# Performance work log

Measured on AMD Instinct MI355X. Metric: run time of the kernel, lower is better.

Reference implementation:

```python
import jax, jax.numpy as jnp
import numpy as np

SHAPES = ((100, 100), (50, 50), (25, 25), (13, 13))
LENS = [h * w for h, w in SHAPES]
STARTS = [0]
for n in LENS[:-1]:
    STARTS.append(STARTS[-1] + n)
S_TOT = sum(LENS)  # 13294
B, C, HH, DH, L, P, NQ, NL, FF = 2, 256, 8, 32, 4, 4, 300, 6, 1024
WH = np.array([[w, h] for h, w in SHAPES], np.float32)  # [L,2] (W,H) offset normalizer


def ln(x, g, b):
    m = x.mean(-1, keepdims=True)
    v = ((x - m) ** 2).mean(-1, keepdims=True)
    return (x - m) * jax.lax.rsqrt(v + 1e-5) * g + b


def bilinear(v, grid):
    # v: [N,Hl,Wl,D]; grid: [N,Q,2] in [-1,1]; grid_sample bilinear, align_corners=False, zero padding
    N, Hl, Wl, Dd = v.shape
    x = (grid[..., 0] + 1.0) * 0.5 * Wl - 0.5
    y = (grid[..., 1] + 1.0) * 0.5 * Hl - 0.5
    x0f = jnp.floor(x); y0f = jnp.floor(y)
    wx = x - x0f; wy = y - y0f
    x0 = x0f.astype(jnp.int32); y0 = y0f.astype(jnp.int32)
    vf = v.reshape(N, Hl * Wl, Dd)
    def g(yi, xi):
        valid = (yi >= 0) & (yi < Hl) & (xi >= 0) & (xi < Wl)
        idx = jnp.clip(yi, 0, Hl - 1) * Wl + jnp.clip(xi, 0, Wl - 1)
        return jnp.take_along_axis(vf, idx[..., None], axis=1) * valid[..., None]
    return (((1 - wy) * (1 - wx))[..., None] * g(y0, x0)
            + ((1 - wy) * wx)[..., None] * g(y0, x0 + 1)
            + (wy * (1 - wx))[..., None] * g(y0 + 1, x0)
            + (wy * wx)[..., None] * g(y0 + 1, x0 + 1))


def msda(query, ref, src, so_w, so_b, aw_w, aw_b, vp_w, vp_b, op_w, op_b):
    # query:[B,Lq,C] ref:[B,Lq,L,2] src:[B,S,C]
    Bq, Lq, _ = query.shape
    value = (src @ vp_w.T + vp_b).reshape(Bq, S_TOT, HH, DH)
    offs = (query @ so_w.T + so_b).reshape(Bq, Lq, HH, L, P, 2)
    aw = jax.nn.softmax((query @ aw_w.T + aw_b).reshape(Bq, Lq, HH, L * P), -1)
    aw = aw.reshape(Bq, Lq, HH, L, P)
    loc = ref[:, :, None, :, None, :] + offs / jnp.asarray(WH)[None, None, None, :, None, :]
    grid = 2.0 * loc - 1.0  # [B,Lq,HH,L,P,2]
    out = jnp.zeros((Bq, HH, Lq, DH), query.dtype)
    for l, (Hl, Wl) in enumerate(SHAPES):
        st = STARTS[l]
        v_l = value[:, st:st + Hl * Wl].reshape(Bq, Hl, Wl, HH, DH).transpose(0, 3, 1, 2, 4).reshape(Bq * HH, Hl, Wl, DH)
        g_l = grid[:, :, :, l].transpose(0, 2, 1, 3, 4).reshape(Bq * HH, Lq * P, 2)
        s = bilinear(v_l, g_l).reshape(Bq, HH, Lq, P, DH)
        out = out + jnp.einsum('bqhp,bhqpd->bhqd', aw[:, :, :, l], s)
    out = out.transpose(0, 2, 1, 3).reshape(Bq, Lq, C)
    return out @ op_w.T + op_b


def enc_ref_points():
    refs = []
    for Hl, Wl in SHAPES:
        ry = (jnp.arange(Hl, dtype=jnp.float32) + 0.5) / Hl
        rx = (jnp.arange(Wl, dtype=jnp.float32) + 0.5) / Wl
        gy, gx = jnp.meshgrid(ry, rx, indexing='ij')
        refs.append(jnp.stack([gx.reshape(-1), gy.reshape(-1)], -1))
    r = jnp.concatenate(refs, 0)  # [S,2]; valid_ratios == 1 (no padding)
    return jnp.broadcast_to(r[None, :, None, :], (B, S_TOT, L, 2))


def _forward(src_flatten, pos_flatten, query_embed, level_embed, refp_w, refp_b,
             eso_w, eso_b, eaw_w, eaw_b, evp_w, evp_b, eop_w, eop_b,
             en1_g, en1_b, el1_w, el1_b, el2_w, el2_b, en2_g, en2_b,
             dso_w, dso_b, daw_w, daw_b, dvp_w, dvp_b, dop_w, dop_b,
             dsa_in_w, dsa_in_b, dsa_out_w, dsa_out_b,
             dn1_g, dn1_b, dn2_g, dn2_b, dn3_g, dn3_b,
             dl1_w, dl1_b, dl2_w, dl2_b):
    lev = jnp.concatenate([jnp.broadcast_to(level_embed[l], (LENS[l], C)) for l in range(L)], 0)
    pos = pos_flatten + lev[None]
    memory = src_flatten
    eref = enc_ref_points()
    for i in range(NL):  # encoder
        q = memory + pos
        m2 = msda(q, eref, memory, eso_w[i], eso_b[i], eaw_w[i], eaw_b[i], evp_w[i], evp_b[i], eop_w[i], eop_b[i])
        memory = ln(memory + m2, en1_g[i], en1_b[i])
        f = jax.nn.relu(memory @ el1_w[i].T + el1_b[i]) @ el2_w[i].T + el2_b[i]
        memory = ln(memory + f, en2_g[i], en2_b[i])
    qpos, tgt = jnp.split(query_embed, 2, axis=-1)
    qpos = jnp.broadcast_to(qpos[None], (B, NQ, C))
    tgt = jnp.broadcast_to(tgt[None], (B, NQ, C))
    ref = jax.nn.sigmoid(qpos @ refp_w.T + refp_b)  # [B,NQ,2]
    init_ref = ref
    ref_in = jnp.broadcast_to(ref[:, :, None, :], (B, NQ, L, 2))
    scale = 1.0 / np.sqrt(DH)
    for i in range(NL):  # decoder
        q = tgt + qpos
        wq, wk, wv = jnp.split(dsa_in_w[i], 3, 0)
        bq, bk, bv = jnp.split(dsa_in_b[i], 3, 0)
        qh = (q @ wq.T + bq).reshape(B, NQ, HH, DH).transpose(0, 2, 1, 3)
        kh = (q @ wk.T + bk).reshape(B, NQ, HH, DH).transpose(0, 2, 1, 3)
        vh = (tgt @ wv.T + bv).reshape(B, NQ, HH, DH).transpose(0, 2, 1, 3)
        att = jax.nn.softmax(jnp.einsum('bhqd,bhkd->bhqk', qh, kh) * scale, -1)
        sa = jnp.einsum('bhqk,bhkd->bhqd', att, vh).transpose(0, 2, 1, 3).reshape(B, NQ, C)
        sa = sa @ dsa_out_w[i].T + dsa_out_b[i]
        tgt = ln(tgt + sa, dn2_g[i], dn2_b[i])
        ca = msda(tgt + qpos, ref_in, memory, dso_w[i], dso_b[i], daw_w[i], daw_b[i], dvp_w[i], dvp_b[i], dop_w[i], dop_b[i])
        tgt = ln(tgt + ca, dn1_g[i], dn1_b[i])
        f = jax.nn.relu(tgt @ dl1_w[i].T + dl1_b[i]) @ dl2_w[i].T + dl2_b[i]
        tgt = ln(tgt + f, dn3_g[i], dn3_b[i])
    return tgt, init_ref, ref


def setup_inputs() -> dict:
    ks = iter(jax.random.split(jax.random.key(0), 80))
    def rn(shape, s=0.02):
        return jax.random.normal(next(ks), shape, jnp.float32) * s
    z = lambda shape: jnp.zeros(shape, jnp.float32)
    o = lambda shape: jnp.ones(shape, jnp.float32)
    HLP2, HLP = HH * L * P * 2, HH * L * P
    return {
        'src_flatten': rn((B, S_TOT, C), 1.0),
        'pos_flatten': rn((B, S_TOT, C), 1.0),
        'query_embed': rn((NQ, 2 * C), 1.0),
        'level_embed': rn((L, C), 1.0),
        'refp_w': rn((2, C)), 'refp_b': z((2,)),
        'eso_w': rn((NL, HLP2, C)), 'eso_b': z((NL, HLP2)),
        'eaw_w': rn((NL, HLP, C)), 'eaw_b': z((NL, HLP)),
        'evp_w': rn((NL, C, C)), 'evp_b': z((NL, C)),
        'eop_w': rn((NL, C, C)), 'eop_b': z((NL, C)),
        'en1_g': o((NL, C)), 'en1_b': z((NL, C)),
        'el1_w': rn((NL, FF, C)), 'el1_b': z((NL, FF)),
        'el2_w': rn((NL, C, FF)), 'el2_b': z((NL, C)),
        'en2_g': o((NL, C)), 'en2_b': z((NL, C)),
        'dso_w': rn((NL, HLP2, C)), 'dso_b': z((NL, HLP2)),
        'daw_w': rn((NL, HLP, C)), 'daw_b': z((NL, HLP)),
        'dvp_w': rn((NL, C, C)), 'dvp_b': z((NL, C)),
        'dop_w': rn((NL, C, C)), 'dop_b': z((NL, C)),
        'dsa_in_w': rn((NL, 3 * C, C)), 'dsa_in_b': z((NL, 3 * C)),
        'dsa_out_w': rn((NL, C, C)), 'dsa_out_b': z((NL, C)),
        'dn1_g': o((NL, C)), 'dn1_b': z((NL, C)),
        'dn2_g': o((NL, C)), 'dn2_b': z((NL, C)),
        'dn3_g': o((NL, C)), 'dn3_b': z((NL, C)),
        'dl1_w': rn((NL, FF, C)), 'dl1_b': z((NL, FF)),
        'dl2_w': rn((NL, C, FF)), 'dl2_b': z((NL, C)),
    }


def reference(src_flatten, pos_flatten, query_embed, level_embed, refp_w, refp_b,
              eso_w, eso_b, eaw_w, eaw_b, evp_w, evp_b, eop_w, eop_b,
              en1_g, en1_b, el1_w, el1_b, el2_w, el2_b, en2_g, en2_b,
              dso_w, dso_b, daw_w, daw_b, dvp_w, dvp_b, dop_w, dop_b,
              dsa_in_w, dsa_in_b, dsa_out_w, dsa_out_b,
              dn1_g, dn1_b, dn2_g, dn2_b, dn3_g, dn3_b,
              dl1_w, dl1_b, dl2_w, dl2_b):
    return _forward(src_flatten, pos_flatten, query_embed, level_embed, refp_w, refp_b,
                    eso_w, eso_b, eaw_w, eaw_b, evp_w, evp_b, eop_w, eop_b,
                    en1_g, en1_b, el1_w, el1_b, el2_w, el2_b, en2_g, en2_b,
                    dso_w, dso_b, daw_w, daw_b, dvp_w, dvp_b, dop_w, dop_b,
                    dsa_in_w, dsa_in_b, dsa_out_w, dsa_out_b,
                    dn1_g, dn1_b, dn2_g, dn2_b, dn3_g, dn3_b,
                    dl1_w, dl1_b, dl2_w, dl2_b)
```

## Files before the change

### kernel.cpp

```cpp
#include <hip/hip_runtime.h>

static constexpr int kS  = 13294;
static constexpr int kB  = 2;
static constexpr int kBS = kB * kS;
static constexpr int kC  = 256;
static constexpr int kH  = 8;
static constexpr int kNQ = 300;
static constexpr int kFF = 1024;
static constexpr int kNL = 6;

using short8 = __attribute__((ext_vector_type(8))) short;
using f32x4  = __attribute__((ext_vector_type(4))) float;

__device__ __forceinline__ unsigned short f2b(float f) {
  unsigned u = __builtin_bit_cast(unsigned, f);
  return (unsigned short)((u + 0x7FFF + ((u >> 16) & 1)) >> 16);
}
__device__ __forceinline__ float bf2f(unsigned short u) {
  return __builtin_bit_cast(float, ((unsigned)u) << 16);
}
__device__ __forceinline__ float bflo(unsigned u) {
  return __builtin_bit_cast(float, u << 16);
}
__device__ __forceinline__ float bfhi(unsigned u) {
  return __builtin_bit_cast(float, u & 0xFFFF0000u);
}

#if defined(__has_builtin)
#if __has_builtin(__builtin_amdgcn_global_load_lds)
#define HAS_GLL 1
#endif
#endif
#ifndef HAS_GLL
#define HAS_GLL 0
#endif

#if HAS_GLL
typedef const __attribute__((address_space(1))) void* gas_t;
typedef __attribute__((address_space(3))) void* las_t;
#define GLOAD16(gp, lp) __builtin_amdgcn_global_load_lds((gas_t)(gp), (las_t)(lp), 16, 0, 0)
#endif


template<int ACT, int OBF>
__global__ __launch_bounds__(256) void gemm_mfma(
    const unsigned short* __restrict__ A, const unsigned short* __restrict__ Wt,
    const float* __restrict__ bias, void* __restrict__ outp, int M, int N, int K) {
  __shared__ __align__(16) unsigned short As[128 * 64];
  __shared__ __align__(16) unsigned short Bs[128 * 64];
  const int t = threadIdx.x;
  const int nB = N >> 7;
  const int tot = gridDim.x;
  const int q8 = tot >> 3, r8 = tot & 7;
  const int xcd = blockIdx.x & 7, pos = blockIdx.x >> 3;
  const int wg = (xcd < r8 ? xcd * (q8 + 1) : r8 * (q8 + 1) + (xcd - r8) * q8) + pos;
  const int m0 = (wg / nB) * 128, n0 = (wg % nB) * 128;
  const int wid = t >> 6, lane = t & 63;
  const int wr = wid >> 1, wc = wid & 1;
  const int srow = t >> 3;
  const int scol = (((t & 7) ^ (srow & 7)) * 8);
  const int lr = lane & 15;
  const int q4 = lane >> 4;
  const int e7 = lr & 7;

  f32x4 acc[4][4];
#pragma unroll
  for (int i = 0; i < 4; ++i)
#pragma unroll
    for (int j = 0; j < 4; ++j) acc[i][j] = (f32x4){0.f, 0.f, 0.f, 0.f};

  for (int k0 = 0; k0 < K; k0 += 64) {
#if HAS_GLL
    __syncthreads();
#pragma unroll
    for (int c = 0; c < 4; ++c) {
      int ar = m0 + c * 32 + srow; if (ar >= M) ar = M - 1;
      GLOAD16(A + (size_t)ar * K + k0 + scol, (char*)As + c * 4096 + t * 16);
      int br = n0 + c * 32 + srow; if (br >= N) br = N - 1;
      GLOAD16(Wt + (size_t)br * K + k0 + scol, (char*)Bs + c * 4096 + t * 16);
    }
    __syncthreads();
#else
    short8 ta[4], tb[4];
#pragma unroll
    for (int c = 0; c < 4; ++c) {
      int ar = m0 + c * 32 + srow; if (ar >= M) ar = M - 1;
      ta[c] = *(const short8*)(A + (size_t)ar * K + k0 + scol);
      int br = n0 + c * 32 + srow; if (br >= N) br = N - 1;
      tb[c] = *(const short8*)(Wt + (size_t)br * K + k0 + scol);
    }
    __syncthreads();
#pragma unroll
    for (int c = 0; c < 4; ++c) {
      *(short8*)&As[c * 2048 + t * 8] = ta[c];
      *(short8*)&Bs[c * 2048 + t * 8] = tb[c];
    }
    __syncthreads();
#endif
#pragma unroll
    for (int kk = 0; kk < 2; ++kk) {
      const int pg = (((kk << 2) + q4) ^ e7) * 8;
      short8 af[4], bf[4];
#pragma unroll
      for (int mi = 0; mi < 4; ++mi)
        af[mi] = *(const short8*)&As[(wr * 64 + mi * 16 + lr) * 64 + pg];
#pragma unroll
      for (int ni = 0; ni < 4; ++ni)
        bf[ni] = *(const short8*)&Bs[(wc * 64 + ni * 16 + lr) * 64 + pg];
#pragma unroll
      for (int mi = 0; mi < 4; ++mi)
#pragma unroll
        for (int ni = 0; ni < 4; ++ni)
          acc[mi][ni] = __builtin_amdgcn_mfma_f32_16x16x32_bf16(af[mi], bf[ni], acc[mi][ni], 0, 0, 0);
    }
  }
  const int orow0 = m0 + wr * 64;
  const int ocol = n0 + wc * 64 + lr;
  float bv[4];
#pragma unroll
  for (int ni = 0; ni < 4; ++ni) bv[ni] = bias[ocol + ni * 16];
#pragma unroll
  for (int mi = 0; mi < 4; ++mi) {
#pragma unroll
    for (int j = 0; j < 4; ++j) {
      const int r = orow0 + mi * 16 + q4 * 4 + j;
      if (r < M) {
#pragma unroll
        for (int ni = 0; ni < 4; ++ni) {
          float v = acc[mi][ni][j] + bv[ni];
          if (ACT) v = fmaxf(v, 0.f);
          if (OBF) ((unsigned short*)outp)[(size_t)r * N + ocol + ni * 16] = f2b(v);
          else     ((float*)outp)[(size_t)r * N + ocol + ni * 16] = v;
        }
      }
    }
  }
}

template<int ACT, int OBF, int CORR>
__global__ __launch_bounds__(256) void gemm_mfma_s(
    const unsigned short* __restrict__ A, const unsigned short* __restrict__ Wt,
    const float* __restrict__ bias, void* __restrict__ outp, int M, int N, int K,
    const float* __restrict__ corr, int cld) {
  __shared__ __align__(16) unsigned short As[64 * 64];
  __shared__ __align__(16) unsigned short Bs[64 * 64];
  const int t = threadIdx.x;
  const int m0 = blockIdx.y * 64, n0 = blockIdx.x * 64;
  const int wid = t >> 6, lane = t & 63;
  const int wr = wid >> 1, wc = wid & 1;
  const int srow = t >> 3;
  const int scol = (((t & 7) ^ (srow & 7)) * 8);
  const int lr = lane & 15;
  const int q4 = lane >> 4;
  const int e7 = lr & 7;

  f32x4 acc[2][2];
#pragma unroll
  for (int i = 0; i < 2; ++i)
#pragma unroll
    for (int j = 0; j < 2; ++j) acc[i][j] = (f32x4){0.f, 0.f, 0.f, 0.f};

  for (int k0 = 0; k0 < K; k0 += 64) {
#if HAS_GLL
    __syncthreads();
#pragma unroll
    for (int c = 0; c < 2; ++c) {
      int ar = m0 + c * 32 + srow; if (ar >= M) ar = M - 1;
      GLOAD16(A + (size_t)ar * K + k0 + scol, (char*)As + c * 4096 + t * 16);
      int br = n0 + c * 32 + srow; if (br >= N) br = N - 1;
      GLOAD16(Wt + (size_t)br * K + k0 + scol, (char*)Bs + c * 4096 + t * 16);
    }
    __syncthreads();
#else
    short8 ta[2], tb[2];
#pragma unroll
    for (int c = 0; c < 2; ++c) {
      int ar = m0 + c * 32 + srow; if (ar >= M) ar = M - 1;
      ta[c] = *(const short8*)(A + (size_t)ar * K + k0 + scol);
      int br = n0 + c * 32 + srow; if (br >= N) br = N - 1;
      tb[c] = *(const short8*)(Wt + (size_t)br * K + k0 + scol);
    }
    __syncthreads();
#pragma unroll
    for (int c = 0; c < 2; ++c) {
      *(short8*)&As[c * 2048 + t * 8] = ta[c];
      *(short8*)&Bs[c * 2048 + t * 8] = tb[c];
    }
    __syncthreads();
#endif
#pragma unroll
    for (int kk = 0; kk < 2; ++kk) {
      const int pg = (((kk << 2) + q4) ^ e7) * 8;
      short8 af[2], bf[2];
#pragma unroll
      for (int mi = 0; mi < 2; ++mi)
        af[mi] = *(const short8*)&As[(wr * 32 + mi * 16 + lr) * 64 + pg];
#pragma unroll
      for (int ni = 0; ni < 2; ++ni)
        bf[ni] = *(const short8*)&Bs[(wc * 32 + ni * 16 + lr) * 64 + pg];
#pragma unroll
      for (int mi = 0; mi < 2; ++mi)
#pragma unroll
        for (int ni = 0; ni < 2; ++ni)
          acc[mi][ni] = __builtin_amdgcn_mfma_f32_16x16x32_bf16(af[mi], bf[ni], acc[mi][ni], 0, 0, 0);
    }
  }
  const int orow0 = m0 + wr * 32;
  const int ocol = n0 + wc * 32 + lr;
  float bv[2];
#pragma unroll
  for (int ni = 0; ni < 2; ++ni) bv[ni] = CORR ? 0.f : bias[ocol + ni * 16];
#pragma unroll
  for (int mi = 0; mi < 2; ++mi) {
#pragma unroll
    for (int j = 0; j < 4; ++j) {
      const int r = orow0 + mi * 16 + q4 * 4 + j;
      if (r < M) {
        const float* cr = CORR ? (corr + (size_t)(r < kNQ ? r : r - kNQ) * cld) : nullptr;
#pragma unroll
        for (int ni = 0; ni < 2; ++ni) {
          float v = acc[mi][ni][j] + (CORR ? cr[ocol + ni * 16] : bv[ni]);
          if (ACT) v = fmaxf(v, 0.f);
          if (OBF) ((unsigned short*)outp)[(size_t)r * N + ocol + ni * 16] = f2b(v);
          else     ((float*)outp)[(size_t)r * N + ocol + ni * 16] = v;
        }
      }
    }
  }
}

template<int WRITEQ, int WRITEF>
__global__ __launch_bounds__(256) void gemm_ln_k(
    const unsigned short* __restrict__ A, const unsigned short* __restrict__ Wt,
    const float* __restrict__ bias, const unsigned short* __restrict__ x_bf,
    const float* __restrict__ g, const float* __restrict__ be,
    float* __restrict__ outf, unsigned short* __restrict__ outb,
    unsigned short* __restrict__ qout, const unsigned short* __restrict__ poslev,
    int M, int K) {
  __shared__ __align__(16) unsigned short As[32 * 128];
  __shared__ __align__(16) unsigned short Bs[256 * 128];
  __shared__ float rsum[32][4], rsq[32][4], rmv[32][2];
  const int t = threadIdx.x;
  const int m0 = blockIdx.x * 32;
  const int wid = t >> 6, lane = t & 63;
  const int lr = lane & 15;
  const int q4 = lane >> 4;
  const int t16 = t >> 4;
  const int g16 = (t & 15) ^ t16;

  f32x4 acc[2][4];
#pragma unroll
  for (int i = 0; i < 2; ++i)
#pragma unroll
    for (int j = 0; j < 4; ++j) acc[i][j] = (f32x4){0.f, 0.f, 0.f, 0.f};

  for (int k0 = 0; k0 < K; k0 += 128) {
#if HAS_GLL
    __syncthreads();
#pragma unroll
    for (int c = 0; c < 2; ++c) {
      int ar = m0 + c * 16 + t16; if (ar >= M) ar = M - 1;
      GLOAD16(A + (size_t)ar * K + k0 + g16 * 8, (char*)As + c * 4096 + t * 16);
    }
#pragma unroll
    for (int c = 0; c < 16; ++c) {
      const int br = c * 16 + t16;
      GLOAD16(Wt + (size_t)br * K + k0 + g16 * 8, (char*)Bs + c * 4096 + t * 16);
    }
    __syncthreads();
#else
    short8 ta[2], tb[16];
#pragma unroll
    for (int c = 0; c < 2; ++c) {
      int ar = m0 + c * 16 + t16; if (ar >= M) ar = M - 1;
      ta[c] = *(const short8*)(A + (size_t)ar * K + k0 + g16 * 8);
    }
#pragma unroll
    for (int c = 0; c < 16; ++c)
      tb[c] = *(const short8*)(Wt + (size_t)(c * 16 + t16) * K + k0 + g16 * 8);
    __syncthreads();
#pragma unroll
    for (int c = 0; c < 2; ++c) *(short8*)&As[c * 2048 + t * 8] = ta[c];
#pragma unroll
    for (int c = 0; c < 16; ++c) *(short8*)&Bs[c * 2048 + t * 8] = tb[c];
    __syncthreads();
#endif
#pragma unroll
    for (int kk = 0; kk < 4; ++kk) {
      const int pg = (((kk << 2) + q4) ^ lr) * 8;
      short8 af[2], bf[4];
#pragma unroll
      for (int mi = 0; mi < 2; ++mi)
        af[mi] = *(const short8*)&As[(mi * 16 + lr) * 128 + pg];
#pragma unroll
      for (int ni = 0; ni < 4; ++ni)
        bf[ni] = *(const short8*)&Bs[(wid * 64 + ni * 16 + lr) * 128 + pg];
#pragma unroll
      for (int mi = 0; mi < 2; ++mi)
#pragma unroll
        for (int ni = 0; ni < 4; ++ni)
          acc[mi][ni] = __builtin_amdgcn_mfma_f32_16x16x32_bf16(af[mi], bf[ni], acc[mi][ni], 0, 0, 0);
    }
  }
  float bv[4], gv[4], bev[4];
  int cols[4];
#pragma unroll
  for (int ni = 0; ni < 4; ++ni) {
    cols[ni] = wid * 64 + ni * 16 + lr;
    bv[ni] = bias[cols[ni]];
    gv[ni] = g[cols[ni]];
    bev[ni] = be[cols[ni]];
  }
#pragma unroll
  for (int mi = 0; mi < 2; ++mi) {
#pragma unroll
    for (int j = 0; j < 4; ++j) {
      const int brow = mi * 16 + q4 * 4 + j;
      int grow = m0 + brow; if (grow >= M) grow = M - 1;
      const unsigned short* xr = x_bf + (size_t)grow * 256;
      float s = 0.f, s2 = 0.f;
#pragma unroll
      for (int ni = 0; ni < 4; ++ni) {
        float v = acc[mi][ni][j] + bv[ni] + bf2f(xr[cols[ni]]);
        acc[mi][ni][j] = v;
        s += v; s2 += v * v;
      }
#pragma unroll
      for (int o = 1; o < 16; o <<= 1) {
        s += __shfl_xor(s, o);
        s2 += __shfl_xor(s2, o);
      }
      if (lr == 0) { rsum[brow][wid] = s; rsq[brow][wid] = s2; }
    }
  }
  __syncthreads();
  if (t < 32) {
    float s = rsum[t][0] + rsum[t][1] + rsum[t][2] + rsum[t][3];
    float s2 = rsq[t][0] + rsq[t][1] + rsq[t][2] + rsq[t][3];
    float mean = s * (1.f / 256.f);
    float var = s2 * (1.f / 256.f) - mean * mean;
    rmv[t][0] = mean;
    rmv[t][1] = rsqrtf(var + 1e-5f);
  }
  __syncthreads();
#pragma unroll
  for (int mi = 0; mi < 2; ++mi) {
#pragma unroll
    for (int j = 0; j < 4; ++j) {
      const int brow = mi * 16 + q4 * 4 + j;
      const int grow = m0 + brow;
      if (grow >= M) continue;
      const float mean = rmv[brow][0], rs = rmv[brow][1];
#pragma unroll
      for (int ni = 0; ni < 4; ++ni) {
        const float v = (acc[mi][ni][j] - mean) * rs * gv[ni] + bev[ni];
        const size_t oi = (size_t)grow * 256 + cols[ni];
        if (WRITEF) outf[oi] = v;
        outb[oi] = f2b(v);
        if (WRITEQ) qout[oi] = f2b(v + bf2f(poslev[oi]));
      }
    }
  }
}

__global__ void cast_bf_k(const float* __restrict__ in, unsigned short* __restrict__ out, int n4) {
  int i = blockIdx.x * 256 + threadIdx.x;
  if (i >= n4) return;
  float4 v = ((const float4*)in)[i];
  ushort4 o; o.x = f2b(v.x); o.y = f2b(v.y); o.z = f2b(v.z); o.w = f2b(v.w);
  ((ushort4*)out)[i] = o;
}

__global__ void pack_soaw_k(const float* __restrict__ so_w, const float* __restrict__ aw_w,
                            unsigned short* __restrict__ out, int total4) {
  int i = blockIdx.x * 256 + threadIdx.x;
  if (i >= total4) return;
  int e = i * 4;
  int l = e / 98304;
  int rem = e - l * 98304;
  int r = rem >> 8;
  int c = rem & 255;
  const float* src = (r < 256) ? (so_w + (size_t)l * 65536 + r * 256 + c)
                               : (aw_w + (size_t)l * 32768 + (r - 256) * 256 + c);
  float4 v = *(const float4*)src;
  ushort4 o; o.x = f2b(v.x); o.y = f2b(v.y); o.z = f2b(v.z); o.w = f2b(v.w);
  ((ushort4*)out)[i] = o;
}

__global__ void pack_bias_k(const float* __restrict__ so_b, const float* __restrict__ aw_b,
                            float* __restrict__ fb) {
  int i = blockIdx.x * 256 + threadIdx.x;
  if (i >= kNL * 384) return;
  int l = i / 384, j = i - l * 384;
  fb[i] = (j < 256) ? so_b[l * 256 + j] : aw_b[l * 128 + j - 256];
}

__global__ void corr_vfix_k(const float* __restrict__ dsa_in_b, float* __restrict__ corr) {
  int i = blockIdx.x * 256 + threadIdx.x;
  if (i >= kNQ * kNL * 256) return;
  int q = i / (kNL * 256);
  int rem = i - q * (kNL * 256);
  int l = rem >> 8, c = rem & 255;
  corr[(size_t)q * (kNL * 768) + l * 768 + 512 + c] = dsa_in_b[l * 768 + 512 + c];
}

__global__ void poslev_k(const float* __restrict__ pos, const float* __restrict__ lev,
                         unsigned short* __restrict__ out, int n4) {
  int i = blockIdx.x * 256 + threadIdx.x;
  if (i >= n4) return;
  int c4 = i & 63;
  int row = i >> 6;
  int s = row % kS;
  int l = (s < 10000) ? 0 : (s < 12500) ? 1 : (s < 13125) ? 2 : 3;
  float4 p = ((const float4*)pos)[i];
  float4 lv = ((const float4*)(lev + l * kC))[c4];
  ushort4 o;
  o.x = f2b(p.x + lv.x); o.y = f2b(p.y + lv.y);
  o.z = f2b(p.z + lv.z); o.w = f2b(p.w + lv.w);
  ((ushort4*)out)[i] = o;
}

__global__ void enc_q_k(const float* __restrict__ src, const unsigned short* __restrict__ poslev,
                        unsigned short* __restrict__ q, int n4) {
  int i = blockIdx.x * 256 + threadIdx.x;
  if (i >= n4) return;
  float4 m = ((const float4*)src)[i];
  ushort4 pl = ((const ushort4*)poslev)[i];
  ushort4 o;
  o.x = f2b(m.x + bf2f(pl.x)); o.y = f2b(m.y + bf2f(pl.y));
  o.z = f2b(m.z + bf2f(pl.z)); o.w = f2b(m.w + bf2f(pl.w));
  ((ushort4*)q)[i] = o;
}

__global__ void refs_k(float* __restrict__ refS) {
  int s = blockIdx.x * 256 + threadIdx.x;
  if (s >= kS) return;
  int st, W;
  if (s < 10000)      { st = 0;     W = 100; }
  else if (s < 12500) { st = 10000; W = 50; }
  else if (s < 13125) { st = 12500; W = 25; }
  else                { st = 13125; W = 13; }
  int idx = s - st;
  int y = idx / W;
  int x = idx - y * W;
  refS[s * 2 + 0] = (x + 0.5f) / (float)W;
  refS[s * 2 + 1] = (y + 0.5f) / (float)W;
}

__global__ __launch_bounds__(256) void msda_fused_k(
    const unsigned short* __restrict__ value, int vstride, int vcol,
    const unsigned short* __restrict__ foab, const float* __restrict__ refs,
    unsigned short* __restrict__ out, int Mq) {
  __shared__ int   sidx[16][2][kH][4];
  __shared__ float sw[16][2][kH][4];
  const int t = threadIdx.x;
  const int bq0 = blockIdx.x * 2;
  const int qq = t >> 7;
  {
    const int bq = bq0 + qq;
    const int b = (bq >= Mq) ? 1 : 0;
    const int qi = bq - b * Mq;
    const int h = (t >> 4) & 7, lp = t & 15, l = lp >> 2;
    const unsigned short* row = foab + (size_t)bq * 384;
    float logit = bf2f(row[256 + h * 16 + lp]);
    float mx = logit;
#pragma unroll
    for (int o = 1; o < 16; o <<= 1) mx = fmaxf(mx, __shfl_xor(mx, o));
    float e = __expf(logit - mx), ssum = e;
#pragma unroll
    for (int o = 1; o < 16; o <<= 1) ssum += __shfl_xor(ssum, o);
    const float a = e / ssum;
    const unsigned opair = *(const unsigned*)(row + h * 32 + lp * 2);
    const float offx = bflo(opair);
    const float offy = bfhi(opair);
    const float rx = refs[qi * 2 + 0];
    const float ry = refs[qi * 2 + 1];
    const int wtab[4] = {100, 50, 25, 13};
    const int stab[4] = {0, 10000, 12500, 13125};
    const int W = wtab[l];
    const int start = stab[l];
    const float px = fmaf(rx, (float)W, offx) - 0.5f;
    const float py = fmaf(ry, (float)W, offy) - 0.5f;
    const float fx = floorf(px), fy = floorf(py);
    const float wx = px - fx, wy = py - fy;
    const int x0 = (int)fx, y0 = (int)fy;
    const int x0c = min(max(x0, 0), W - 1);
    const int x1c = min(max(x0 + 1, 0), W - 1);
    const int y0c = min(max(y0, 0), W - 1);
    const int y1c = min(max(y0 + 1, 0), W - 1);
    const float vx0 = (x0 >= 0 && x0 < W) ? 1.f : 0.f;
    const float vx1 = (x0 + 1 >= 0 && x0 + 1 < W) ? 1.f : 0.f;
    const float vy0 = (y0 >= 0 && y0 < W) ? 1.f : 0.f;
    const float vy1 = (y0 + 1 >= 0 && y0 + 1 < W) ? 1.f : 0.f;
    const int base0 = b * kS * vstride + vcol + start * vstride;
    sidx[lp][qq][h][0] = base0 + (y0c * W + x0c) * vstride;
    sidx[lp][qq][h][1] = base0 + (y0c * W + x1c) * vstride;
    sidx[lp][qq][h][2] = base0 + (y1c * W + x0c) * vstride;
    sidx[lp][qq][h][3] = base0 + (y1c * W + x1c) * vstride;
    const float omwx = 1.f - wx, omwy = 1.f - wy;
    sw[lp][qq][h][0] = a * omwy * omwx * vy0 * vx0;
    sw[lp][qq][h][1] = a * omwy * wx * vy0 * vx1;
    sw[lp][qq][h][2] = a * wy * omwx * vy1 * vx0;
    sw[lp][qq][h][3] = a * wy * wx * vy1 * vx1;
  }
  __syncthreads();
  const int h = (t >> 4) & 7, dp = t & 15;
  const int bq = bq0 + qq;
  const int chan = h * 64 + dp * 4;
  const char* valc = (const char*)value;
  float aLo0 = 0.f, aLo1 = 0.f, aHi0 = 0.f, aHi1 = 0.f;
#pragma unroll
  for (int p0 = 0; p0 < 16; p0 += 8) {
    unsigned u[32];
    float w[32];
#pragma unroll
    for (int pp = 0; pp < 8; ++pp) {
      const int4 I = *(const int4*)&sidx[p0 + pp][qq][h][0];
      const float4 Wv = *(const float4*)&sw[p0 + pp][qq][h][0];
      u[pp * 4 + 0] = *(const unsigned*)(valc + (unsigned)(I.x + chan));
      u[pp * 4 + 1] = *(const unsigned*)(valc + (unsigned)(I.y + chan));
      u[pp * 4 + 2] = *(const unsigned*)(valc + (unsigned)(I.z + chan));
      u[pp * 4 + 3] = *(const unsigned*)(valc + (unsigned)(I.w + chan));
      w[pp * 4 + 0] = Wv.x; w[pp * 4 + 1] = Wv.y;
      w[pp * 4 + 2] = Wv.z; w[pp * 4 + 3] = Wv.w;
    }
#pragma unroll
    for (int j = 0; j < 32; j += 2) {
      aLo0 = fmaf(w[j], bflo(u[j]), aLo0);
      aHi0 = fmaf(w[j], bfhi(u[j]), aHi0);
      aLo1 = fmaf(w[j + 1], bflo(u[j + 1]), aLo1);
      aHi1 = fmaf(w[j + 1], bfhi(u[j + 1]), aHi1);
    }
  }
  const float accLo = aLo0 + aLo1;
  const float accHi = aHi0 + aHi1;
  const unsigned packed = (unsigned)f2b(accLo) | ((unsigned)f2b(accHi) << 16);
  ((unsigned*)out)[(size_t)bq * 128 + h * 16 + dp] = packed;
}

__global__ void dec_init_k(const float* __restrict__ qe, float* __restrict__ tgt,
                           unsigned short* __restrict__ tgt_bf, float* __restrict__ qposb,
                           unsigned short* __restrict__ qpos_bf) {
  int i = blockIdx.x * 256 + threadIdx.x;
  if (i >= kNQ * kC) return;
  int q = i >> 8, c = i & 255;
  float qp = qe[q * 512 + c];
  qposb[i] = qp;
  qpos_bf[i] = f2b(qp);
  float tg = qe[q * 512 + 256 + c];
  tgt[i] = tg;
  tgt[kNQ * kC + i] = tg;
  unsigned short tb = f2b(tg);
  tgt_bf[i] = tb;
  tgt_bf[kNQ * kC + i] = tb;
}

__global__ __launch_bounds__(64) void ref_k(const float* __restrict__ qposb,
                                            const float* __restrict__ rw,
                                            const float* __restrict__ rb,
                                            float* __restrict__ ref300) {
  const int q = blockIdx.x;
  const int lane = threadIdx.x;
  const float4 qv = ((const float4*)(qposb + q * 256))[lane];
  const float4 w0 = ((const float4*)rw)[lane];
  const float4 w1 = ((const float4*)(rw + 256))[lane];
  float a0 = qv.x * w0.x + qv.y * w0.y + qv.z * w0.z + qv.w * w0.w;
  float a1 = qv.x * w1.x + qv.y * w1.y + qv.z * w1.z + qv.w * w1.w;
#pragma unroll
  for (int off = 32; off; off >>= 1) {
    a0 += __shfl_xor(a0, off);
    a1 += __shfl_xor(a1, off);
  }
  if (lane == 0) {
    ref300[q * 2 + 0] = 1.f / (1.f + __expf(-(a0 + rb[0])));
    ref300[q * 2 + 1] = 1.f / (1.f + __expf(-(a1 + rb[1])));
  }
}

__global__ __launch_bounds__(64) void dec_attn_k(const float* __restrict__ qkv,
                                                 unsigned short* __restrict__ outp) {
  const int bid = blockIdx.x;
  const int q = bid % kNQ;
  const int bh = bid / kNQ;
  const int h = bh & 7;
  const int b = bh >> 3;
  const int lane = threadIdx.x;
  __shared__ float p[304];
  const float* qv = qkv + (size_t)(b * kNQ + q) * 768 + h * 32;
  float qreg[32];
#pragma unroll
  for (int m = 0; m < 32; ++m) qreg[m] = qv[m];
  float scores[5];
  float mx = -1e30f;
#pragma unroll
  for (int j = 0; j < 5; ++j) {
    const int k = lane + j * 64;
    float sc = -1e30f;
    if (k < kNQ) {
      const float* kv = qkv + (size_t)(b * kNQ + k) * 768 + 256 + h * 32;
      float acc = 0.f;
#pragma unroll
      for (int m = 0; m < 32; ++m) acc = fmaf(qreg[m], kv[m], acc);
      sc = acc * 0.17677669529663687f;
    }
    scores[j] = sc;
    mx = fmaxf(mx, sc);
  }
#pragma unroll
  for (int off = 32; off; off >>= 1) mx = fmaxf(mx, __shfl_xor(mx, off));
  float sum = 0.f;
#pragma unroll
  for (int j = 0; j < 5; ++j) {
    const int k = lane + j * 64;
    float e = 0.f;
    if (k < kNQ) e = __expf(scores[j] - mx);
    scores[j] = e;
    sum += e;
  }
#pragma unroll
  for (int off = 32; off; off >>= 1) sum += __shfl_xor(sum, off);
  const float inv = 1.f / sum;
#pragma unroll
  for (int j = 0; j < 5; ++j) {
    const int k = lane + j * 64;
    if (k < kNQ) p[k] = scores[j] * inv;
  }
  __syncthreads();
  const int d = lane & 31, half = lane >> 5;
  float acc = 0.f;
  for (int k = half * 150; k < half * 150 + 150; ++k)
    acc = fmaf(p[k], qkv[(size_t)(b * kNQ + k) * 768 + 512 + h * 32 + d], acc);
  acc += __shfl_down(acc, 32);
  if (lane < 32) outp[((size_t)(b * kNQ + q)) * 256 + h * 32 + d] = f2b(acc);
}

__global__ void write_refs_k(const float* __restrict__ ref300, float* __restrict__ outp) {
  int i = blockIdx.x * 256 + threadIdx.x;
  if (i >= 1200) return;
  float v = ref300[i % 600];
  outp[153600 + i] = v;
  outp[154800 + i] = v;
}

__global__ void sentinel_k(float* __restrict__ outp) {
  if (threadIdx.x < 64) outp[threadIdx.x] = 12345.0f;
}

extern "C" void kernel_launch(void* const* d_in, const int* in_sizes, int n_in,
                              void* d_out, int out_size, void* d_ws, size_t ws_size,
                              hipStream_t stream) {
  const float* src      = (const float*)d_in[0];
  const float* pos      = (const float*)d_in[1];
  const float* qe       = (const float*)d_in[2];
  const float* lev      = (const float*)d_in[3];
  const float* refp_w   = (const float*)d_in[4];
  const float* refp_b   = (const float*)d_in[5];
  const float* eso_w    = (const float*)d_in[6];
  const float* eso_b    = (const float*)d_in[7];
  const float* eaw_w    = (const float*)d_in[8];
  const float* eaw_b    = (const float*)d_in[9];
  const float* evp_w    = (const float*)d_in[10];
  const float* evp_b    = (const float*)d_in[11];
  const float* eop_w    = (const float*)d_in[12];
  const float* eop_b    = (const float*)d_in[13];
  const float* en1_g    = (const float*)d_in[14];
  const float* en1_b    = (const float*)d_in[15];
  const float* el1_w    = (const float*)d_in[16];
  const float* el1_b    = (const float*)d_in[17];
  const float* el2_w    = (const float*)d_in[18];
  const float* el2_b    = (const float*)d_in[19];
  const float* en2_g    = (const float*)d_in[20];
  const float* en2_b    = (const float*)d_in[21];
  const float* dso_w    = (const float*)d_in[22];
  const float* dso_b    = (const float*)d_in[23];
  const float* daw_w    = (const float*)d_in[24];
  const float* daw_b    = (const float*)d_in[25];
  const float* dvp_w    = (const float*)d_in[26];
  const float* dvp_b    = (const float*)d_in[27];
  const float* dop_w    = (const float*)d_in[28];
  const float* dop_b    = (const float*)d_in[29];
  const float* dsa_in_w = (const float*)d_in[30];
  const float* dsa_in_b = (const float*)d_in[31];
  const float* dsa_out_w= (const float*)d_in[32];
  const float* dsa_out_b= (const float*)d_in[33];
  const float* dn1_g    = (const float*)d_in[34];
  const float* dn1_b    = (const float*)d_in[35];
  const float* dn2_g    = (const float*)d_in[36];
  const float* dn2_b    = (const float*)d_in[37];
  const float* dn3_g    = (const float*)d_in[38];
  const float* dn3_b    = (const float*)d_in[39];
  const float* dl1_w    = (const float*)d_in[40];
  const float* dl1_b    = (const float*)d_in[41];
  const float* dl2_w    = (const float*)d_in[42];
  const float* dl2_b    = (const float*)d_in[43];

  float* Wsp = (float*)d_ws;
  size_t off = 0;
  auto alloc = [&](size_t n) { float* p = Wsp + off; off += n; return p; };
  const size_t NBC = (size_t)kBS * kC;
  unsigned short* memory_bf = (unsigned short*)alloc(NBC / 2);
  unsigned short* poslev_bf = (unsigned short*)alloc(NBC / 2);
  float* r2       = alloc(NBC);
  unsigned short* val_bf = (unsigned short*)r2;
  float* r3       = alloc(NBC / 2);
  unsigned short* qbuf_bf = (unsigned short*)r3;
  unsigned short* sampbuf_bf = (unsigned short*)r3;
  float* r4       = alloc(NBC * 2);
  unsigned short* foab_bf = (unsigned short*)r4;
  unsigned short* hid_bf = (unsigned short*)r4;
  unsigned short* val_all = (unsigned short*)r2;
  float* refS     = alloc((size_t)kS * 2 + 2);
  auto allocb = [&](size_t elems) { return (unsigned short*)alloc(elems / 2); };
  unsigned short* fesoawW = allocb((size_t)kNL * 384 * 256);
  unsigned short* evpW  = allocb((size_t)kNL * 65536);
  unsigned short* eopW  = allocb((size_t)kNL * 65536);
  unsigned short* el1W  = allocb((size_t)kNL * 262144);
  unsigned short* el2W  = allocb((size_t)kNL * 262144);
  unsigned short* fdsoawW = allocb((size_t)kNL * 384 * 256);
  unsigned short* dvpW  = allocb((size_t)kNL * 65536);
  unsigned short* dopW  = allocb((size_t)kNL * 65536);
  unsigned short* dsaiW = allocb((size_t)kNL * 196608);
  unsigned short* dsaoW = allocb((size_t)kNL * 65536);
  unsigned short* dl1W  = allocb((size_t)kNL * 262144);
  unsigned short* dl2W  = allocb((size_t)kNL * 262144);
  float* fbias_e  = alloc((size_t)kNL * 384);
  float* fbias_d  = alloc((size_t)kNL * 384);
  const size_t NQC = (size_t)kB * kNQ * kC;
  float* tgt      = alloc(NQC);
  unsigned short* tgt_bf = (unsigned short*)alloc(NQC / 2);
  float* qposb    = alloc((size_t)kNQ * kC);
  unsigned short* qpos_bf = (unsigned short*)alloc((size_t)kNQ * kC / 2);
  float* qkvbuf   = alloc((size_t)kB * kNQ * 768);
  unsigned short* sabuf_bf = (unsigned short*)alloc(NQC / 2);
  unsigned short* dfoab_bf = (unsigned short*)alloc((size_t)kB * kNQ * 384 / 2);
  unsigned short* dsamp_bf = (unsigned short*)alloc(NQC / 2);
  unsigned short* dffnh_bf = (unsigned short*)alloc((size_t)kB * kNQ * kFF / 2);
  float* corrQKV  = alloc((size_t)kNQ * kNL * 768);
  float* corrSOAW = alloc((size_t)kNQ * kNL * 384);
  float* ref300   = alloc(600);

  if (ws_size < off * sizeof(float)) {
    hipLaunchKernelGGL(sentinel_k, dim3(1), dim3(64), 0, stream, (float*)d_out);
    return;
  }

  auto GEMM = [&](const unsigned short* A, const unsigned short* Wt, const float* bias,
                  void* out, int M, int N, int K, int variant) {
    dim3 g((N / 128) * ((M + 127) / 128));
    if (variant == 1)
      hipLaunchKernelGGL((gemm_mfma<1, 1>), g, dim3(256), 0, stream, A, Wt, bias, out, M, N, K);
    else if (variant == 2)
      hipLaunchKernelGGL((gemm_mfma<0, 1>), g, dim3(256), 0, stream, A, Wt, bias, out, M, N, K);
    else
      hipLaunchKernelGGL((gemm_mfma<0, 0>), g, dim3(256), 0, stream, A, Wt, bias, out, M, N, K);
  };
  auto CASTW = [&](const float* srcw, unsigned short* dstw, size_t elems) {
    int n4 = (int)(elems / 4);
    hipLaunchKernelGGL(cast_bf_k, dim3((n4 + 255) / 256), dim3(256), 0, stream, srcw, dstw, n4);
  };

  {
    const int tot4 = kNL * 98304 / 4;
    hipLaunchKernelGGL(pack_soaw_k, dim3((tot4 + 255) / 256), dim3(256), 0, stream,
                       eso_w, eaw_w, fesoawW, tot4);
    hipLaunchKernelGGL(pack_soaw_k, dim3((tot4 + 255) / 256), dim3(256), 0, stream,
                       dso_w, daw_w, fdsoawW, tot4);
  }
  CASTW(evp_w, evpW, (size_t)kNL * 65536);
  CASTW(eop_w, eopW, (size_t)kNL * 65536);
  CASTW(el1_w, el1W, (size_t)kNL * 262144);
  CASTW(el2_w, el2W, (size_t)kNL * 262144);
  CASTW(dvp_w, dvpW, (size_t)kNL * 65536);
  CASTW(dop_w, dopW, (size_t)kNL * 65536);
  CASTW(dsa_in_w, dsaiW, (size_t)kNL * 196608);
  CASTW(dsa_out_w, dsaoW, (size_t)kNL * 65536);
  CASTW(dl1_w, dl1W, (size_t)kNL * 262144);
  CASTW(dl2_w, dl2W, (size_t)kNL * 262144);
  hipLaunchKernelGGL(pack_bias_k, dim3((kNL * 384 + 255) / 256), dim3(256), 0, stream,
                     eso_b, eaw_b, fbias_e);
  hipLaunchKernelGGL(pack_bias_k, dim3((kNL * 384 + 255) / 256), dim3(256), 0, stream,
                     dso_b, daw_b, fbias_d);
  const int n4full = kBS * 64;
  hipLaunchKernelGGL(cast_bf_k, dim3((n4full + 255) / 256), dim3(256), 0, stream,
                     src, memory_bf, n4full);
  hipLaunchKernelGGL(poslev_k, dim3((n4full + 255) / 256), dim3(256), 0, stream,
                     pos, lev, poslev_bf, n4full);
  hipLaunchKernelGGL(refs_k, dim3((kS + 255) / 256), dim3(256), 0, stream, refS);
  hipLaunchKernelGGL(enc_q_k, dim3((n4full + 255) / 256), dim3(256), 0, stream,
                     src, poslev_bf, qbuf_bf, n4full);

  const int grid_ln = (kBS + 31) / 32;
  for (int i = 0; i < kNL; ++i) {
    GEMM(memory_bf, evpW + (size_t)i * 65536, evp_b + i * kC, val_bf, kBS, 256, 256, 2);
    GEMM(qbuf_bf, fesoawW + (size_t)i * 98304, fbias_e + i * 384, foab_bf, kBS, 384, 256, 2);
    hipLaunchKernelGGL(msda_fused_k, dim3(kBS / 2), dim3(256), 0, stream,
                       val_bf, 512, 0, foab_bf, refS, sampbuf_bf, kS);
    hipLaunchKernelGGL((gemm_ln_k<0, 0>), dim3(grid_ln), dim3(256), 0, stream,
                       sampbuf_bf, eopW + (size_t)i * 65536, eop_b + i * kC,
                       memory_bf, en1_g + i * kC, en1_b + i * kC,
                       (float*)nullptr, memory_bf, (unsigned short*)nullptr,
                       (const unsigned short*)nullptr, kBS, 256);
    GEMM(memory_bf, el1W + (size_t)i * 262144, el1_b + i * kFF, hid_bf, kBS, 1024, 256, 1);
    hipLaunchKernelGGL((gemm_ln_k<1, 0>), dim3(grid_ln), dim3(256), 0, stream,
                       hid_bf, el2W + (size_t)i * 262144, el2_b + i * kC,
                       memory_bf, en2_g + i * kC, en2_b + i * kC,
                       (float*)nullptr, memory_bf, qbuf_bf, poslev_bf, kBS, 1024);
  }

  hipLaunchKernelGGL(dec_init_k, dim3(300), dim3(256), 0, stream, qe, tgt, tgt_bf, qposb, qpos_bf);
  hipLaunchKernelGGL(ref_k, dim3(kNQ), dim3(64), 0, stream, qposb, refp_w, refp_b, ref300);
  GEMM(memory_bf, dvpW, dvp_b, val_all, kBS, kNL * 256, 256, 2);
  hipLaunchKernelGGL((gemm_mfma_s<0, 0, 0>), dim3(kNL * 768 / 64, (kNQ + 63) / 64), dim3(256), 0,
                     stream, qpos_bf, dsaiW, dsa_in_b, corrQKV, kNQ, kNL * 768, 256,
                     (const float*)nullptr, 0);
  hipLaunchKernelGGL(corr_vfix_k, dim3((kNQ * kNL * 256 + 255) / 256), dim3(256), 0, stream,
                     dsa_in_b, corrQKV);
  hipLaunchKernelGGL((gemm_mfma_s<0, 0, 0>), dim3(kNL * 384 / 64, (kNQ + 63) / 64), dim3(256), 0,
                     stream, qpos_bf, fdsoawW, fbias_d, corrSOAW, kNQ, kNL * 384, 256,
                     (const float*)nullptr, 0);

  const int MD = kB * kNQ;
  const int grid_lnd = (MD + 31) / 32;
  for (int i = 0; i < kNL; ++i) {
    hipLaunchKernelGGL((gemm_mfma_s<0, 0, 1>), dim3(768 / 64, (MD + 63) / 64), dim3(256), 0,
                       stream, tgt_bf, dsaiW + (size_t)i * 196608, (const float*)nullptr,
                       qkvbuf, MD, 768, 256, corrQKV + (size_t)i * 768, kNL * 768);
    hipLaunchKernelGGL(dec_attn_k, dim3(kB * kH * kNQ), dim3(64), 0, stream,
                       qkvbuf, sabuf_bf);
    hipLaunchKernelGGL((gemm_ln_k<0, 1>), dim3(grid_lnd), dim3(256), 0, stream,
                       sabuf_bf, dsaoW + (size_t)i * 65536, dsa_out_b + i * kC,
                       tgt_bf, dn2_g + i * kC, dn2_b + i * kC,
                       tgt, tgt_bf, (unsigned short*)nullptr,
                       (const unsigned short*)nullptr, MD, 256);
    hipLaunchKernelGGL((gemm_mfma_s<0, 1, 1>), dim3(384 / 64, (MD + 63) / 64), dim3(256), 0,
                       stream, tgt_bf, fdsoawW + (size_t)i * 98304, (const float*)nullptr,
                       dfoab_bf, MD, 384, 256, corrSOAW + (size_t)i * 384, kNL * 384);
    hipLaunchKernelGGL(msda_fused_k, dim3(MD / 2), dim3(256), 0, stream,
                       val_all, kNL * 512, i * 512, dfoab_bf, ref300, dsamp_bf, kNQ);
    hipLaunchKernelGGL((gemm_ln_k<0, 1>), dim3(grid_lnd), dim3(256), 0, stream,
                       dsamp_bf, dopW + (size_t)i * 65536, dop_b + i * kC,
                       tgt_bf, dn1_g + i * kC, dn1_b + i * kC,
                       tgt, tgt_bf, (unsigned short*)nullptr,
                       (const unsigned short*)nullptr, MD, 256);
    hipLaunchKernelGGL((gemm_mfma_s<1, 1, 0>), dim3(1024 / 64, (MD + 63) / 64), dim3(256), 0,
                       stream, tgt_bf, dl1W + (size_t)i * 262144, dl1_b + i * kFF,
                       dffnh_bf, MD, 1024, 256, (const float*)nullptr, 0);
    hipLaunchKernelGGL((gemm_ln_k<0, 1>), dim3(grid_lnd), dim3(256), 0, stream,
                       dffnh_bf, dl2W + (size_t)i * 262144, dl2_b + i * kC,
                       tgt_bf, dn3_g + i * kC, dn3_b + i * kC,
                       tgt, tgt_bf, (unsigned short*)nullptr,
                       (const unsigned short*)nullptr, MD, 1024);
  }

  hipMemcpyAsync(d_out, tgt, NQC * sizeof(float), hipMemcpyDeviceToDevice, stream);
  hipLaunchKernelGGL(write_refs_k, dim3(5), dim3(256), 0, stream, ref300, (float*)d_out);
}
```

Measured before the change: 1.694 ms.

## Double-buffer LDS tiles in fused GEMM+LayerNorm kernel with BK=64

Restructures the gemm_ln_k main loop to use two 64-wide K stages in shared memory. The next tile is prefetched while MFMAs run on the current one, with a single barrier per iteration. The swizzle is reworked for the narrower tiles. This targets load latency exposed by the previous load-sync-compute pattern, at the cost of more iterations. In the non-GLL path, the synchronous load-store into the other buffer may give limited real overlap.

```diff
diff --git a/kernel.cpp b/kernel.cpp
--- a/kernel.cpp
+++ b/kernel.cpp
@@ -237,16 +237,20 @@
     float* __restrict__ outf, unsigned short* __restrict__ outb,
     unsigned short* __restrict__ qout, const unsigned short* __restrict__ poslev,
     int M, int K) {
-  __shared__ __align__(16) unsigned short As[32 * 128];
-  __shared__ __align__(16) unsigned short Bs[256 * 128];
+  __shared__ __align__(16) unsigned short As[2][32 * 64];
+  __shared__ __align__(16) unsigned short Bs[2][256 * 64];
   __shared__ float rsum[32][4], rsq[32][4], rmv[32][2];
   const int t = threadIdx.x;
   const int m0 = blockIdx.x * 32;
   const int wid = t >> 6, lane = t & 63;
   const int lr = lane & 15;
   const int q4 = lane >> 4;
-  const int t16 = t >> 4;
-  const int g16 = (t & 15) ^ t16;
+  const int srow = t >> 3;
+  const int scol = (((t & 7) ^ (srow & 7)) * 8);
+  const int e7 = lr & 7;
+
+  int arow = m0 + srow; if (arow >= M) arow = M - 1;
+  const unsigned short* Arow = A + (size_t)arow * K;
 
   f32x4 acc[2][4];
 #pragma unroll
@@ -254,54 +258,53 @@
 #pragma unroll
     for (int j = 0; j < 4; ++j) acc[i][j] = (f32x4){0.f, 0.f, 0.f, 0.f};
 
-  for (int k0 = 0; k0 < K; k0 += 128) {
+  auto STAGE = [&](int buf, int k0) {
 #if HAS_GLL
-    __syncthreads();
-#pragma unroll
-    for (int c = 0; c < 2; ++c) {
-      int ar = m0 + c * 16 + t16; if (ar >= M) ar = M - 1;
-      GLOAD16(A + (size_t)ar * K + k0 + g16 * 8, (char*)As + c * 4096 + t * 16);
-    }
-#pragma unroll
-    for (int c = 0; c < 16; ++c) {
-      const int br = c * 16 + t16;
-      GLOAD16(Wt + (size_t)br * K + k0 + g16 * 8, (char*)Bs + c * 4096 + t * 16);
-    }
-    __syncthreads();
+    GLOAD16(Arow + k0 + scol, (char*)As[buf] + t * 16);
+#pragma unroll
+    for (int c = 0; c < 8; ++c) {
+      const int br = c * 32 + srow;
+      GLOAD16(Wt + (size_t)br * K + k0 + scol, (char*)Bs[buf] + c * 4096 + t * 16);
+    }
 #else
-    short8 ta[2], tb[16];
-#pragma unroll
-    for (int c = 0; c < 2; ++c) {
-      int ar = m0 + c * 16 + t16; if (ar >= M) ar = M - 1;
-      ta[c] = *(const short8*)(A + (size_t)ar * K + k0 + g16 * 8);
-    }
-#pragma unroll
-    for (int c = 0; c < 16; ++c)
-      tb[c] = *(const short8*)(Wt + (size_t)(c * 16 + t16) * K + k0 + g16 * 8);
-    __syncthreads();
-#pragma unroll
-    for (int c = 0; c < 2; ++c) *(short8*)&As[c * 2048 + t * 8] = ta[c];
-#pragma unroll
-    for (int c = 0; c < 16; ++c) *(short8*)&Bs[c * 2048 + t * 8] = tb[c];
-    __syncthreads();
+    {
+      short8 ta = *(const short8*)(Arow + k0 + scol);
+      *(short8*)&As[buf][t * 8] = ta;
+#pragma unroll
+      for (int c = 0; c < 8; ++c) {
+        short8 tb = *(const short8*)(Wt + (size_t)(c * 32 + srow) * K + k0 + scol);
+        *(short8*)&Bs[buf][c * 2048 + t * 8] = tb;
+      }
+    }
 #endif
-#pragma unroll
-    for (int kk = 0; kk < 4; ++kk) {
-      const int pg = (((kk << 2) + q4) ^ lr) * 8;
+  };
+
+  const int ntiles = K >> 6;
+  STAGE(0, 0);
+  __syncthreads();
+  int cur = 0;
+  for (int tt = 0; tt < ntiles; ++tt) {
+    if (tt + 1 < ntiles) STAGE(cur ^ 1, (tt + 1) * 64);
+#pragma unroll
+    for (int kk = 0; kk < 2; ++kk) {
+      const int pg = (((kk << 2) + q4) ^ e7) * 8;
       short8 af[2], bf[4];
 #pragma unroll
       for (int mi = 0; mi < 2; ++mi)
-        af[mi] = *(const short8*)&As[(mi * 16 + lr) * 128 + pg];
+        af[mi] = *(const short8*)&As[cur][(mi * 16 + lr) * 64 + pg];
 #pragma unroll
       for (int ni = 0; ni < 4; ++ni)
-        bf[ni] = *(const short8*)&Bs[(wid * 64 + ni * 16 + lr) * 128 + pg];
+        bf[ni] = *(const short8*)&Bs[cur][(wid * 64 + ni * 16 + lr) * 64 + pg];
 #pragma unroll
       for (int mi = 0; mi < 2; ++mi)
 #pragma unroll
         for (int ni = 0; ni < 4; ++ni)
           acc[mi][ni] = __builtin_amdgcn_mfma_f32_16x16x32_bf16(af[mi], bf[ni], acc[mi][ni], 0, 0, 0);
     }
-  }
+    __syncthreads();
+    cur ^= 1;
+  }
+
   float bv[4], gv[4], bev[4];
   int cols[4];
 #pragma unroll
```

New measurement: 1.787 ms. 1.05x slower.
